# Optimization experiments

Measured on AMD Instinct MI355X. Metric: run time of the kernel, lower is better.

The kernel has to match this reference:

```python
import jax, jax.numpy as jnp
import numpy as np

BATCH, BITS, HID = 65536, 64, 512
EPS = 1e-5

# M[s, i, j] = 1 if j == i - s  (left-shift-by-s permutation, causal)
_SHIFT_M = jnp.asarray(
    (np.arange(BITS)[None, :, None] - np.arange(BITS)[:, None, None]
     == np.arange(BITS)[None, None, :]).astype(np.float32))


def _layernorm(x, g, b):
    m = jnp.mean(x, axis=-1, keepdims=True)
    v = jnp.var(x, axis=-1, keepdims=True)
    return (x - m) * jax.lax.rsqrt(v + EPS) * g + b


def setup_inputs() -> dict:
    key = jax.random.key(0)
    ks = jax.random.split(key, 8)
    inp = {
        'a_bits': jax.random.uniform(ks[0], (BATCH, BITS), dtype=jnp.float32),
        'shift_bits': jax.random.uniform(ks[1], (BATCH, BITS), dtype=jnp.float32),
        # shift_decoder params: Linear(64,512) -> LN -> GELU -> Linear(512,512) -> LN -> GELU -> Linear(512,64)
        'W1': jax.random.normal(ks[2], (BITS, HID), dtype=jnp.float32) * (1.0 / np.sqrt(BITS)),
        'b1': jnp.zeros((HID,), jnp.float32),
        'g1': jnp.ones((HID,), jnp.float32),
        'be1': jnp.zeros((HID,), jnp.float32),
        'W2': jax.random.normal(ks[3], (HID, HID), dtype=jnp.float32) * (1.0 / np.sqrt(HID)),
        'b2': jnp.zeros((HID,), jnp.float32),
        'g2': jnp.ones((HID,), jnp.float32),
        'be2': jnp.zeros((HID,), jnp.float32),
        'W3': jax.random.normal(ks[4], (HID, BITS), dtype=jnp.float32) * (1.0 / np.sqrt(HID)),
        'b3': jnp.zeros((BITS,), jnp.float32),
    }
    return inp


def reference(a_bits, shift_bits, W1, b1, g1, be1, W2, b2, g2, be2, W3, b3):
    temperature = jnp.float32(1.0)
    # shift decoder MLP
    h = jax.nn.gelu(_layernorm(shift_bits @ W1 + b1, g1, be1), approximate=False)
    h = jax.nn.gelu(_layernorm(h @ W2 + b2, g2, be2), approximate=False)
    shift_logits = (h @ W3 + b3)[:, :BITS]
    # training path: soft shift distribution
    shift_probs = jax.nn.softmax(shift_logits / temperature, axis=-1)
    # weighted permutation matrix, then batched matvec (faithful to einsum+bmm)
    M_weighted = jnp.einsum('bs,sij->bij', shift_probs, _SHIFT_M)
    output = jnp.einsum('bij,bj->bi', M_weighted, a_bits)
    return output
```

## Files before the change

kernel.cpp:

```cpp
#include <hip/hip_runtime.h>
#include <hip/hip_bf16.h>
#include <math.h>

#define BATCH 65536
#define NT 512
#define BM 32

using f32x4 = __attribute__((ext_vector_type(4))) float;
using s16x8 = __attribute__((ext_vector_type(8))) short;

#define MFMA16(a, b, c) __builtin_amdgcn_mfma_f32_16x16x32_bf16((a), (b), (c), 0, 0, 0)

__device__ __forceinline__ unsigned short f2bf(float f) {
    unsigned u = __builtin_bit_cast(unsigned, f);
    u = u + 0x7FFFu + ((u >> 16) & 1u);
    return (unsigned short)(u >> 16);
}

__device__ __forceinline__ float fast_erf(float x) {
    float ax = fabsf(x);
    float t = __builtin_amdgcn_rcpf(fmaf(0.3275911f, ax, 1.0f));
    float poly = t * fmaf(t, fmaf(t, fmaf(t, fmaf(t, 1.061405429f, -1.453152027f),
                                          1.421413741f), -0.284496736f), 0.254829592f);
    float r = 1.0f - poly * __expf(-ax * ax);
    return copysignf(r, x);
}
__device__ __forceinline__ float gelu(float y) {
    return 0.5f * y * (1.0f + fast_erf(y * 0.70710678118654752f));
}

__device__ __forceinline__ int hswz(int row, int k) {
    return row * 1024 + ((((k >> 3) ^ (row & 7))) << 4) + ((k & 7) << 1);
}
__device__ __forceinline__ int xaddr(int base, int row, int k) {
    return base + row * 128 + ((((k >> 3) ^ (row & 7))) << 4) + ((k & 7) << 1);
}

__global__ void weights_frag(const float* __restrict__ W1, const float* __restrict__ W2,
                             const float* __restrict__ W3, unsigned short* __restrict__ wt) {
    int b = blockIdx.x;
    int lane = threadIdx.x;
    const float* src; unsigned short* dst; int N, fragidx;
    if (b < 64)       { src = W1; dst = wt;          N = 512; fragidx = b; }
    else if (b < 576) { src = W2; dst = wt + 32768;  N = 512; fragidx = b - 64; }
    else              { src = W3; dst = wt + 294912; N = 64;  fragidx = b - 576; }
    int nt, ks;
    if (b < 64) { nt = fragidx >> 1; ks = fragidx & 1; }
    else        { nt = fragidx >> 4; ks = fragidx & 15; }
    int n  = nt * 16 + (lane & 15);
    int k0 = ks * 32 + (lane >> 4) * 8;
    unsigned short o[8];
#pragma unroll
    for (int e = 0; e < 8; e++) o[e] = f2bf(src[(size_t)(k0 + e) * N + n]);
    *(uint4*)(dst + ((size_t)fragidx * 64 + lane) * 8) = *(uint4*)o;
}

__device__ __forceinline__ void ln_partials(f32x4 (&acc)[2][4], char* smem, int redb,
                                            int ln, int g, int wave) {
#pragma unroll
    for (int fm = 0; fm < 2; fm++)
#pragma unroll
        for (int r = 0; r < 4; r++) {
            float s = 0.f, q = 0.f;
#pragma unroll
            for (int fn = 0; fn < 4; fn++) { float v = acc[fm][fn][r]; s += v; q += v * v; }
#pragma unroll
            for (int m = 1; m < 16; m <<= 1) { s += __shfl_xor(s, m, 64); q += __shfl_xor(q, m, 64); }
            if (ln == 0) {
                int row = fm * 16 + g * 4 + r;
                float* rp = (float*)(smem + redb + (row * 8 + wave) * 8);
                rp[0] = s; rp[1] = q;
            }
        }
}

#define SMEM_K1 39168
__global__ __launch_bounds__(NT, 6) void k1_gemm1(
    const float* __restrict__ shift_bits,
    const float* __restrict__ b1, const float* __restrict__ g1, const float* __restrict__ be1,
    const unsigned short* __restrict__ wt, unsigned short* __restrict__ h1,
    int rowoff) {
    __shared__ char smem[SMEM_K1];
    const int t = threadIdx.x;
    const int wave = t >> 6, lane = t & 63, g = lane >> 4, ln = lane & 15;
    const int row0 = rowoff + blockIdx.x * BM;
    const int lrow0 = blockIdx.x * BM;
    const int n0w = wave * 64;
    const int XB = 32768, RB = 36864, SB = 38912;
    const unsigned short* wt1f = wt;

    {
        int r = t >> 4, c = t & 15;
        float4 x = *(const float4*)(shift_bits + (size_t)(row0 + r) * 64 + c * 4);
        unsigned p0 = (unsigned)f2bf(x.x) | ((unsigned)f2bf(x.y) << 16);
        unsigned p1 = (unsigned)f2bf(x.z) | ((unsigned)f2bf(x.w) << 16);
        uint2 v; v.x = p0; v.y = p1;
        *(uint2*)(smem + XB + r * 128 + (((c >> 1) ^ (r & 7)) << 4) + (c & 1) * 8) = v;
    }
    __syncthreads();

    f32x4 acc[2][4];
#pragma unroll
    for (int fm = 0; fm < 2; fm++)
#pragma unroll
        for (int fn = 0; fn < 4; fn++) acc[fm][fn] = (f32x4){0.f, 0.f, 0.f, 0.f};
#pragma unroll
    for (int ks = 0; ks < 2; ks++) {
        s16x8 af[2], bf[4];
#pragma unroll
        for (int fn = 0; fn < 4; fn++) {
            int fragidx = (wave * 4 + fn) * 2 + ks;
            bf[fn] = *(const s16x8*)(wt1f + ((size_t)fragidx * 64 + lane) * 8);
        }
#pragma unroll
        for (int fm = 0; fm < 2; fm++)
            af[fm] = *(const s16x8*)(smem + xaddr(XB, fm * 16 + ln, ks * 32 + g * 8));
#pragma unroll
        for (int fm = 0; fm < 2; fm++)
#pragma unroll
            for (int fn = 0; fn < 4; fn++) acc[fm][fn] = MFMA16(af[fm], bf[fn], acc[fm][fn]);
    }

    {
        float bb[4];
#pragma unroll
        for (int fn = 0; fn < 4; fn++) bb[fn] = b1[n0w + fn * 16 + ln];
#pragma unroll
        for (int fm = 0; fm < 2; fm++)
#pragma unroll
            for (int fn = 0; fn < 4; fn++)
#pragma unroll
                for (int r = 0; r < 4; r++) acc[fm][fn][r] += bb[fn];
    }
    ln_partials(acc, smem, RB, ln, g, wave);
    __syncthreads();
    if (t < 32) {
        float s = 0.f, q = 0.f;
#pragma unroll
        for (int w = 0; w < 8; w++) {
            float* rp = (float*)(smem + RB + (t * 8 + w) * 8);
            s += rp[0]; q += rp[1];
        }
        float mu = s * (1.0f / 512.0f);
        float var = q * (1.0f / 512.0f) - mu * mu;
        float rs = rsqrtf(var + 1e-5f);
        float* sp = (float*)(smem + SB + t * 8);
        sp[0] = mu; sp[1] = rs;
    }
    __syncthreads();
    {
        float gm[4], bt[4];
#pragma unroll
        for (int fn = 0; fn < 4; fn++) { int c = n0w + fn * 16 + ln; gm[fn] = g1[c]; bt[fn] = be1[c]; }
#pragma unroll
        for (int fm = 0; fm < 2; fm++)
#pragma unroll
            for (int r = 0; r < 4; r++) {
                int row = fm * 16 + g * 4 + r;
                float* sp = (float*)(smem + SB + row * 8);
                float mu = sp[0], rs = sp[1];
#pragma unroll
                for (int fn = 0; fn < 4; fn++) {
                    int col = n0w + fn * 16 + ln;
                    float y = (acc[fm][fn][r] - mu) * rs * gm[fn] + bt[fn];
                    *(unsigned short*)(smem + hswz(row, col)) = f2bf(gelu(y));
                }
            }
    }
    __syncthreads();
    {
        int r = t >> 4, c0 = (t & 15) * 32;
        unsigned short* dst = h1 + (size_t)(lrow0 + r) * 512 + c0;
#pragma unroll
        for (int j = 0; j < 4; j++) {
            int gr = (c0 >> 3) + j;
            uint4 v = *(const uint4*)(smem + r * 1024 + ((gr ^ (r & 7)) << 4));
            *(uint4*)(dst + j * 8) = v;
        }
    }
}

#define SMEM_K23 35072
__global__ __launch_bounds__(NT, 4) void k23_fused(
    const unsigned short* __restrict__ h1, const float* __restrict__ a_bits,
    const float* __restrict__ b2, const float* __restrict__ g2, const float* __restrict__ be2,
    const float* __restrict__ b3, const unsigned short* __restrict__ wt,
    float* __restrict__ out, int rowoff) {
    __shared__ char smem[SMEM_K23];
    const int t = threadIdx.x;
    const int wave = t >> 6, lane = t & 63, g = lane >> 4, ln = lane & 15;
    const int lrow0 = blockIdx.x * BM;
    const int row0 = rowoff + lrow0;
    const int RB = 32768, SB = 34816;
    const unsigned short* wt2f = wt + 32768;
    const unsigned short* wt3f = wt + 294912;

    {
        int r = t >> 4, c0 = (t & 15) * 32;
        const unsigned short* src = h1 + (size_t)(lrow0 + r) * 512 + c0;
#pragma unroll
        for (int j = 0; j < 4; j++) {
            uint4 v = *(const uint4*)(src + j * 8);
            int gr = (c0 >> 3) + j;
            *(uint4*)(smem + r * 1024 + ((gr ^ (r & 7)) << 4)) = v;
        }
    }

    const int n0w = wave * 64;
    const unsigned short* bp[4];
#pragma unroll
    for (int fn = 0; fn < 4; fn++)
        bp[fn] = wt2f + ((size_t)(wave * 4 + fn) * 16 * 64 + lane) * 8;

    __syncthreads();

    f32x4 acc[2][4];
#pragma unroll
    for (int fm = 0; fm < 2; fm++)
#pragma unroll
        for (int fn = 0; fn < 4; fn++) acc[fm][fn] = (f32x4){0.f, 0.f, 0.f, 0.f};
    {
        s16x8 bcur[4], bnxt[4];
#pragma unroll
        for (int fn = 0; fn < 4; fn++) bcur[fn] = *(const s16x8*)(bp[fn]);
#pragma unroll
        for (int step = 0; step < 16; step++) {
            if (step < 15) {
#pragma unroll
                for (int fn = 0; fn < 4; fn++)
                    bnxt[fn] = *(const s16x8*)(bp[fn] + (size_t)(step + 1) * 512);
            }
            s16x8 af[2];
#pragma unroll
            for (int fm = 0; fm < 2; fm++)
                af[fm] = *(const s16x8*)(smem + hswz(fm * 16 + ln, step * 32 + g * 8));
#pragma unroll
            for (int fm = 0; fm < 2; fm++)
#pragma unroll
                for (int fn = 0; fn < 4; fn++) acc[fm][fn] = MFMA16(af[fm], bcur[fn], acc[fm][fn]);
#pragma unroll
            for (int fn = 0; fn < 4; fn++) bcur[fn] = bnxt[fn];
        }
    }

    {
        float bb[4];
#pragma unroll
        for (int fn = 0; fn < 4; fn++) bb[fn] = b2[n0w + fn * 16 + ln];
#pragma unroll
        for (int fm = 0; fm < 2; fm++)
#pragma unroll
            for (int fn = 0; fn < 4; fn++)
#pragma unroll
                for (int r = 0; r < 4; r++) acc[fm][fn][r] += bb[fn];
    }
    ln_partials(acc, smem, RB, ln, g, wave);
    __syncthreads();
    if (t < 32) {
        float s = 0.f, q = 0.f;
#pragma unroll
        for (int w = 0; w < 8; w++) {
            float* rp = (float*)(smem + RB + (t * 8 + w) * 8);
            s += rp[0]; q += rp[1];
        }
        float mu = s * (1.0f / 512.0f);
        float var = q * (1.0f / 512.0f) - mu * mu;
        float rs = rsqrtf(var + 1e-5f);
        float* sp = (float*)(smem + SB + t * 8);
        sp[0] = mu; sp[1] = rs;
    }
    __syncthreads();

    {
        float gm[4], bt[4];
#pragma unroll
        for (int fn = 0; fn < 4; fn++) { int c = n0w + fn * 16 + ln; gm[fn] = g2[c]; bt[fn] = be2[c]; }
#pragma unroll
        for (int fm = 0; fm < 2; fm++)
#pragma unroll
            for (int r = 0; r < 4; r++) {
                int row = fm * 16 + g * 4 + r;
                float* sp = (float*)(smem + SB + row * 8);
                float mu = sp[0], rs = sp[1];
#pragma unroll
                for (int fn = 0; fn < 4; fn++) {
                    int col = n0w + fn * 16 + ln;
                    float y = (acc[fm][fn][r] - mu) * rs * gm[fn] + bt[fn];
                    *(unsigned short*)(smem + hswz(row, col)) = f2bf(gelu(y));
                }
            }
    }
    __syncthreads();

    const int mh = wave >> 2, q = wave & 3;
    float b3v = b3[q * 16 + ln];
    const unsigned short* b3p = wt3f + ((size_t)q * 16 * 64 + lane) * 8;
    f32x4 acc3a = (f32x4){0.f, 0.f, 0.f, 0.f};
    f32x4 acc3b = (f32x4){0.f, 0.f, 0.f, 0.f};
#pragma unroll
    for (int ks = 0; ks < 16; ks += 2) {
        s16x8 bfr0 = *(const s16x8*)(b3p + (size_t)ks * 512);
        s16x8 bfr1 = *(const s16x8*)(b3p + (size_t)(ks + 1) * 512);
        s16x8 af0 = *(const s16x8*)(smem + hswz(mh * 16 + ln, ks * 32 + g * 8));
        s16x8 af1 = *(const s16x8*)(smem + hswz(mh * 16 + ln, (ks + 1) * 32 + g * 8));
        acc3a = MFMA16(af0, bfr0, acc3a);
        acc3b = MFMA16(af1, bfr1, acc3b);
    }
    __syncthreads();

    const int LOGB = 0, ABUF = 8704, LST = 272, AST = 544;
#pragma unroll
    for (int r = 0; r < 4; r++) {
        int row = mh * 16 + g * 4 + r;
        *(float*)(smem + LOGB + row * LST + (q * 16 + ln) * 4) = acc3a[r] + acc3b[r] + b3v;
    }
    {
        int r = t >> 4, c0 = (t & 15) * 4;
        float* ap = (float*)(smem + ABUF + r * AST);
        float4 z4 = {0.f, 0.f, 0.f, 0.f};
        *(float4*)(ap + c0) = z4;
        float4 av = *(const float4*)(a_bits + (size_t)(row0 + r) * 64 + c0);
        *(float4*)(ap + 64 + c0) = av;
    }
    __syncthreads();

    {
        int r = t >> 4, c0 = (t & 15) * 4;
        float* lp = (float*)(smem + LOGB + r * LST + c0 * 4);
        float4 v = *(float4*)lp;
        float mx = fmaxf(fmaxf(v.x, v.y), fmaxf(v.z, v.w));
#pragma unroll
        for (int d = 1; d < 16; d <<= 1) mx = fmaxf(mx, __shfl_xor(mx, d, 64));
        float e0 = __expf(v.x - mx), e1 = __expf(v.y - mx);
        float e2 = __expf(v.z - mx), e3 = __expf(v.w - mx);
        float s = e0 + e1 + e2 + e3;
#pragma unroll
        for (int d = 1; d < 16; d <<= 1) s += __shfl_xor(s, d, 64);
        float inv = 1.0f / s;
        float4 o; o.x = e0 * inv; o.y = e1 * inv; o.z = e2 * inv; o.w = e3 * inv;
        *(float4*)lp = o;
    }
    __syncthreads();

    {
        int r = t >> 4, i0 = (t & 15) * 4;
        const float* prow = (const float*)(smem + LOGB + r * LST);
        const float* apad = (const float*)(smem + ABUF + r * AST);
        float W[8];
        {
            float4 wa = *(const float4*)(apad + i0 + 60);
            float4 wb = *(const float4*)(apad + i0 + 64);
            W[0] = wa.x; W[1] = wa.y; W[2] = wa.z; W[3] = wa.w;
            W[4] = wb.x; W[5] = wb.y; W[6] = wb.z; W[7] = wb.w;
        }
        float o0 = 0.f, o1 = 0.f, o2 = 0.f, o3 = 0.f;
#pragma unroll
        for (int s4 = 0; s4 < 16; s4++) {
            float4 p4 = *(const float4*)(prow + 4 * s4);
            o0 = fmaf(p4.x, W[4], fmaf(p4.y, W[3], fmaf(p4.z, W[2], fmaf(p4.w, W[1], o0))));
            o1 = fmaf(p4.x, W[5], fmaf(p4.y, W[4], fmaf(p4.z, W[3], fmaf(p4.w, W[2], o1))));
            o2 = fmaf(p4.x, W[6], fmaf(p4.y, W[5], fmaf(p4.z, W[4], fmaf(p4.w, W[3], o2))));
            o3 = fmaf(p4.x, W[7], fmaf(p4.y, W[6], fmaf(p4.z, W[5], fmaf(p4.w, W[4], o3))));
            if (s4 < 15) {
                W[4] = W[0]; W[5] = W[1]; W[6] = W[2]; W[7] = W[3];
                float4 nw = *(const float4*)(apad + i0 + 56 - 4 * s4);
                W[0] = nw.x; W[1] = nw.y; W[2] = nw.z; W[3] = nw.w;
            }
        }
        float4 o; o.x = o0; o.y = o1; o.z = o2; o.w = o3;
        *(float4*)(out + (size_t)(row0 + r) * 64 + i0) = o;
    }
}

extern "C" void kernel_launch(void* const* d_in, const int* in_sizes, int n_in,
                              void* d_out, int out_size, void* d_ws, size_t ws_size,
                              hipStream_t stream) {
    const float* a_bits = (const float*)d_in[0];
    const float* shift  = (const float*)d_in[1];
    const float* W1  = (const float*)d_in[2];
    const float* b1  = (const float*)d_in[3];
    const float* g1  = (const float*)d_in[4];
    const float* be1 = (const float*)d_in[5];
    const float* W2  = (const float*)d_in[6];
    const float* b2  = (const float*)d_in[7];
    const float* g2  = (const float*)d_in[8];
    const float* be2 = (const float*)d_in[9];
    const float* W3  = (const float*)d_in[10];
    const float* b3  = (const float*)d_in[11];
    float* out = (float*)d_out;

    char* ws = (char*)d_ws;
    unsigned short* wt = (unsigned short*)ws;

    int CH = 1;
    while (CH < 32) {
        size_t need = 655360ull + 1024ull * (size_t)(BATCH / CH);
        if (need <= ws_size) break;
        CH *= 2;
    }
    const int chunk = BATCH / CH;
    unsigned short* h1 = (unsigned short*)(ws + 655360);

    weights_frag<<<640, 64, 0, stream>>>(W1, W2, W3, wt);
    for (int c = 0; c < CH; c++) {
        int rowoff = c * chunk;
        k1_gemm1<<<chunk / BM, NT, 0, stream>>>(shift, b1, g1, be1, wt, h1, rowoff);
        k23_fused<<<chunk / BM, NT, 0, stream>>>(h1, a_bits, b2, g2, be2, b3, wt, out, rowoff);
    }
}
```

Measured before the change: 144.3 us.

## Fuse first MLP layer kernel with second/third layer kernel, drop h1 buffer

Merges the layer-1 GEMM+LN+GELU kernel into the layer-2/3 kernel so the bf16 hidden activation stays in shared memory rather than round-tripping through a global workspace buffer. Also removes the chunked launch loop, leaving one fused launch over the whole batch. The fused kernel uses launch bounds of 4 blocks per CU instead of 6 for the first stage, which may reduce occupancy for the layer-1 portion.

```diff
diff --git a/kernel.cpp b/kernel.cpp
--- a/kernel.cpp
+++ b/kernel.cpp
@@ -74,20 +74,22 @@
         }
 }
 
-#define SMEM_K1 39168
-__global__ __launch_bounds__(NT, 6) void k1_gemm1(
-    const float* __restrict__ shift_bits,
+#define SMEM_K123 39168
+__global__ __launch_bounds__(NT, 4) void k123_fused(
+    const float* __restrict__ shift_bits, const float* __restrict__ a_bits,
     const float* __restrict__ b1, const float* __restrict__ g1, const float* __restrict__ be1,
-    const unsigned short* __restrict__ wt, unsigned short* __restrict__ h1,
-    int rowoff) {
-    __shared__ char smem[SMEM_K1];
+    const float* __restrict__ b2, const float* __restrict__ g2, const float* __restrict__ be2,
+    const float* __restrict__ b3, const unsigned short* __restrict__ wt,
+    float* __restrict__ out) {
+    __shared__ char smem[SMEM_K123];
     const int t = threadIdx.x;
     const int wave = t >> 6, lane = t & 63, g = lane >> 4, ln = lane & 15;
-    const int row0 = rowoff + blockIdx.x * BM;
-    const int lrow0 = blockIdx.x * BM;
+    const int row0 = blockIdx.x * BM;
     const int n0w = wave * 64;
     const int XB = 32768, RB = 36864, SB = 38912;
     const unsigned short* wt1f = wt;
+    const unsigned short* wt2f = wt + 32768;
+    const unsigned short* wt3f = wt + 294912;
 
     {
         int r = t >> 4, c = t & 15;
@@ -168,53 +170,11 @@
             }
     }
     __syncthreads();
-    {
-        int r = t >> 4, c0 = (t & 15) * 32;
-        unsigned short* dst = h1 + (size_t)(lrow0 + r) * 512 + c0;
-#pragma unroll
-        for (int j = 0; j < 4; j++) {
-            int gr = (c0 >> 3) + j;
-            uint4 v = *(const uint4*)(smem + r * 1024 + ((gr ^ (r & 7)) << 4));
-            *(uint4*)(dst + j * 8) = v;
-        }
-    }
-}
-
-#define SMEM_K23 35072
-__global__ __launch_bounds__(NT, 4) void k23_fused(
-    const unsigned short* __restrict__ h1, const float* __restrict__ a_bits,
-    const float* __restrict__ b2, const float* __restrict__ g2, const float* __restrict__ be2,
-    const float* __restrict__ b3, const unsigned short* __restrict__ wt,
-    float* __restrict__ out, int rowoff) {
-    __shared__ char smem[SMEM_K23];
-    const int t = threadIdx.x;
-    const int wave = t >> 6, lane = t & 63, g = lane >> 4, ln = lane & 15;
-    const int lrow0 = blockIdx.x * BM;
-    const int row0 = rowoff + lrow0;
-    const int RB = 32768, SB = 34816;
-    const unsigned short* wt2f = wt + 32768;
-    const unsigned short* wt3f = wt + 294912;
-
-    {
-        int r = t >> 4, c0 = (t & 15) * 32;
-        const unsigned short* src = h1 + (size_t)(lrow0 + r) * 512 + c0;
-#pragma unroll
-        for (int j = 0; j < 4; j++) {
-            uint4 v = *(const uint4*)(src + j * 8);
-            int gr = (c0 >> 3) + j;
-            *(uint4*)(smem + r * 1024 + ((gr ^ (r & 7)) << 4)) = v;
-        }
-    }
-
-    const int n0w = wave * 64;
+
     const unsigned short* bp[4];
 #pragma unroll
     for (int fn = 0; fn < 4; fn++)
         bp[fn] = wt2f + ((size_t)(wave * 4 + fn) * 16 * 64 + lane) * 8;
-
-    __syncthreads();
-
-    f32x4 acc[2][4];
 #pragma unroll
     for (int fm = 0; fm < 2; fm++)
 #pragma unroll
@@ -270,7 +230,6 @@
         sp[0] = mu; sp[1] = rs;
     }
     __syncthreads();
-
     {
         float gm[4], bt[4];
 #pragma unroll
@@ -388,23 +347,9 @@
     const float* W3  = (const float*)d_in[10];
     const float* b3  = (const float*)d_in[11];
     float* out = (float*)d_out;
-
-    char* ws = (char*)d_ws;
-    unsigned short* wt = (unsigned short*)ws;
-
-    int CH = 1;
-    while (CH < 32) {
-        size_t need = 655360ull + 1024ull * (size_t)(BATCH / CH);
-        if (need <= ws_size) break;
-        CH *= 2;
-    }
-    const int chunk = BATCH / CH;
-    unsigned short* h1 = (unsigned short*)(ws + 655360);
+    unsigned short* wt = (unsigned short*)d_ws;
 
     weights_frag<<<640, 64, 0, stream>>>(W1, W2, W3, wt);
-    for (int c = 0; c < CH; c++) {
-        int rowoff = c * chunk;
-        k1_gemm1<<<chunk / BM, NT, 0, stream>>>(shift, b1, g1, be1, wt, h1, rowoff);
-        k23_fused<<<chunk / BM, NT, 0, stream>>>(h1, a_bits, b2, g2, be2, b3, wt, out, rowoff);
-    }
-}
+    k123_fused<<<BATCH / BM, NT, 0, stream>>>(shift, a_bits, b1, g1, be1,
+                                              b2, g2, be2, b3, wt, out);
+}
```

After: 142.3 us. Within noise of the previous version (-1.4%).
